# Optimization experiments

Measured on AMD Instinct MI355X. Metric: run time of the kernel, lower is better.

The kernel has to match this reference:

```python
import jax, jax.numpy as jnp
import numpy as np

N_NODES = 65536
IN_CH = 512
HIDDEN = 256          # hidden_channels[0] == encoder_hidden
OUT_CH = 8
NUM_GRAPHS = 32
MAX_LEN = 4096        # static pad bound (>= max per-graph length)
BN_EPS = 1e-5


def _make_batch_ids():
    # deterministic ragged per-graph lengths summing exactly to N_NODES
    rng = np.random.RandomState(0)
    d = rng.randint(-512, 512, size=NUM_GRAPHS)
    d[-1] -= d.sum()
    lengths = N_NODES // NUM_GRAPHS + d          # each in ~[1536, 2560] <= MAX_LEN
    return jnp.asarray(np.repeat(np.arange(NUM_GRAPHS), lengths), dtype=jnp.int32)


def setup_inputs() -> dict:
    key = jax.random.key(0)
    ks = jax.random.split(key, 12)
    f32 = jnp.float32
    inp = {
        'x_res': jax.random.normal(ks[0], (N_NODES, IN_CH), dtype=f32),
        'batch': _make_batch_ids(),
        # BatchNorm1d affine params
        'bn_gamma': jnp.ones((IN_CH,), f32),
        'bn_beta': jnp.zeros((IN_CH,), f32),
        # input2transformer: Linear(C,2H) GELU Linear(2H,H) GELU Linear(H,H)
        'W1': jax.random.normal(ks[1], (IN_CH, 2 * HIDDEN), f32) * (1.0 / np.sqrt(IN_CH)),
        'b1': jnp.zeros((2 * HIDDEN,), f32),
        'W2': jax.random.normal(ks[2], (2 * HIDDEN, HIDDEN), f32) * (1.0 / np.sqrt(2 * HIDDEN)),
        'b2': jnp.zeros((HIDDEN,), f32),
        'W3': jax.random.normal(ks[3], (HIDDEN, HIDDEN), f32) * (1.0 / np.sqrt(HIDDEN)),
        'b3': jnp.zeros((HIDDEN,), f32),
        # out_angles: Linear(encoder_hidden, out_ch) GELU DynamicTanh Tanh
        'Wo': jax.random.normal(ks[4], (HIDDEN, OUT_CH), f32) * (1.0 / np.sqrt(HIDDEN)),
        'bo': jnp.zeros((OUT_CH,), f32),
        'dyt_alpha': jnp.asarray(0.5, f32),
        'dyt_w': jnp.ones((OUT_CH,), f32),
        'dyt_b': jnp.zeros((OUT_CH,), f32),
    }
    return inp


def _forward(x_res, batch, bn_gamma, bn_beta, W1, b1, W2, b2, W3, b3,
             Wo, bo, dyt_alpha, dyt_w, dyt_b):
    # BatchNorm1d (training-mode batch stats, biased var), dropout is identity (eval)
    mu = jnp.mean(x_res, axis=0)
    var = jnp.mean((x_res - mu) ** 2, axis=0)
    x = (x_res - mu) * jax.lax.rsqrt(var + BN_EPS) * bn_gamma + bn_beta
    # input2transformer MLP (torch GELU default = exact erf)
    gelu = lambda t: jax.nn.gelu(t, approximate=False)
    x = gelu(x @ W1 + b1)
    x = gelu(x @ W2 + b2)
    x = x @ W3 + b3                                   # [N, HIDDEN]
    # ragged -> padded: scatter each node into (graph, position-in-graph)
    counts = jax.ops.segment_sum(jnp.ones_like(batch, dtype=jnp.int32), batch,
                                 num_segments=NUM_GRAPHS)
    offsets = jnp.concatenate([jnp.zeros((1,), jnp.int32),
                               jnp.cumsum(counts)[:-1].astype(jnp.int32)])
    pos = jnp.arange(N_NODES, dtype=jnp.int32) - offsets[batch]
    x_pad = jnp.zeros((NUM_GRAPHS, MAX_LEN, HIDDEN), x.dtype).at[batch, pos].set(x)
    z = jnp.transpose(x_pad, (1, 0, 2))               # [MAX_LEN, NUM_GRAPHS, HIDDEN] (stack dim=1)
    # out_angles head: Linear -> GELU -> DynamicTanh -> Tanh
    a = gelu(z @ Wo + bo)
    a = dyt_w * jnp.tanh(dyt_alpha * a) + dyt_b       # DynamicTanh (channels_last)
    return jnp.tanh(a)                                # [MAX_LEN, NUM_GRAPHS, OUT_CH]


def reference(x_res, batch, bn_gamma, bn_beta, W1, b1, W2, b2, W3, b3,
              Wo, bo, dyt_alpha, dyt_w, dyt_b):
    return _forward(x_res, batch, bn_gamma, bn_beta, W1, b1, W2, b2, W3, b3,
                    Wo, bo, dyt_alpha, dyt_w, dyt_b)
```

## Files before the change

kernel.cpp:

```cpp
#include <hip/hip_runtime.h>
#include <hip/hip_bf16.h>

#define N_NODES 65536
#define IN_CH 512
#define HIDDEN 256
#define OUT_CH 8
#define NUM_GRAPHS 32
#define MAX_LEN 4096
#define BN_EPS 1e-5f
#define BN_BLOCKS 2048

using short8  = __attribute__((ext_vector_type(8))) short;
using floatx4 = __attribute__((ext_vector_type(4))) float;
typedef unsigned int u32;
typedef unsigned short u16;

__device__ inline u16 f2b(float f) {
    u32 u = __float_as_uint(f);
    u += 0x7FFFu + ((u >> 16) & 1u);
    return (u16)(u >> 16);
}
__device__ inline float gelu_f(float x) {
    float z = x + 0.044715f * x * x * x;
    float e = __builtin_exp2f(-2.3022078f * z);
    return x * __builtin_amdgcn_rcpf(1.0f + e);
}
__device__ inline float tanh_f(float y) {
    y = fminf(fmaxf(y, -20.0f), 20.0f);
    float t = __builtin_exp2f(2.885390082f * y);
    return (t - 1.0f) * __builtin_amdgcn_rcpf(t + 1.0f);
}
__device__ inline void load_lds16(const void* g, void* l) {
    __builtin_amdgcn_global_load_lds(
        (const __attribute__((address_space(1))) u32*)g,
        (__attribute__((address_space(3))) u32*)l, 16, 0, 0);
}

__global__ __launch_bounds__(256) void statscast_k(const float* __restrict__ x,
                                                   u16* __restrict__ xb,
                                                   float4* __restrict__ partials) {
    __shared__ float4 sS[128];
    __shared__ float4 sQ[128];
    int tid = threadIdx.x;
    int half = tid >> 7;
    int c = tid & 127;
    const float4* x4 = (const float4*)x;
    uint2* xb2 = (uint2*)xb;
    float4 s = make_float4(0.f, 0.f, 0.f, 0.f);
    float4 q = make_float4(0.f, 0.f, 0.f, 0.f);
    int row0 = blockIdx.x * 32;
#pragma unroll
    for (int r = half; r < 32; r += 2) {
        size_t off = (size_t)(row0 + r) * 128 + c;
        float4 v = x4[off];
        s.x += v.x; s.y += v.y; s.z += v.z; s.w += v.w;
        q.x += v.x * v.x; q.y += v.y * v.y; q.z += v.z * v.z; q.w += v.w * v.w;
        uint2 o;
        o.x = (u32)f2b(v.x) | ((u32)f2b(v.y) << 16);
        o.y = (u32)f2b(v.z) | ((u32)f2b(v.w) << 16);
        xb2[off] = o;
    }
    if (half == 1) { sS[c] = s; sQ[c] = q; }
    __syncthreads();
    if (half == 0) {
        float4 s2 = sS[c], q2 = sQ[c];
        s.x += s2.x; s.y += s2.y; s.z += s2.z; s.w += s2.w;
        q.x += q2.x; q.y += q2.y; q.z += q2.z; q.w += q2.w;
        partials[(size_t)blockIdx.x * 256 + c * 2]     = make_float4(s.x, q.x, s.y, q.y);
        partials[(size_t)blockIdx.x * 256 + c * 2 + 1] = make_float4(s.z, q.z, s.w, q.w);
    }
}

__global__ __launch_bounds__(256) void bn_reduce_k(const float4* __restrict__ partials,
                                                   const float* __restrict__ gamma,
                                                   const float* __restrict__ beta,
                                                   float* __restrict__ scale,
                                                   float* __restrict__ shift) {
    __shared__ float4 sd[256];
    int tid = threadIdx.x;
    int g = blockIdx.x;
    float4 a = make_float4(0.f, 0.f, 0.f, 0.f);
    for (int r = tid; r < BN_BLOCKS; r += 256) {
        float4 v = partials[(size_t)r * 256 + g];
        a.x += v.x; a.y += v.y; a.z += v.z; a.w += v.w;
    }
    sd[tid] = a;
    __syncthreads();
    for (int st = 128; st > 0; st >>= 1) {
        if (tid < st) {
            float4 b = sd[tid + st];
            float4 m = sd[tid];
            m.x += b.x; m.y += b.y; m.z += b.z; m.w += b.w;
            sd[tid] = m;
        }
        __syncthreads();
    }
    if (tid == 0) {
        float4 t = sd[0];
        int c0 = g * 2, c1 = g * 2 + 1;
        const float inv = 1.0f / N_NODES;
        float mu0 = t.x * inv, var0 = t.y * inv - mu0 * mu0;
        float mu1 = t.z * inv, var1 = t.w * inv - mu1 * mu1;
        float sc0 = gamma[c0] * rsqrtf(var0 + BN_EPS);
        float sc1 = gamma[c1] * rsqrtf(var1 + BN_EPS);
        scale[c0] = sc0; shift[c0] = beta[c0] - mu0 * sc0;
        scale[c1] = sc1; shift[c1] = beta[c1] - mu1 * sc1;
    }
}

__global__ __launch_bounds__(256) void prep_k(const float* __restrict__ W1,
                                              const float* __restrict__ W2,
                                              const float* __restrict__ W3,
                                              const float* __restrict__ b1,
                                              const float* __restrict__ scale,
                                              const float* __restrict__ shift,
                                              u16* __restrict__ W1T,
                                              u16* __restrict__ W2T,
                                              u16* __restrict__ W3T,
                                              float* __restrict__ b1f,
                                              const int* __restrict__ batch,
                                              int* __restrict__ offsets,
                                              const float* __restrict__ bo,
                                              const float* __restrict__ alpha_p,
                                              const float* __restrict__ dyt_w,
                                              const float* __restrict__ dyt_b,
                                              float* __restrict__ out) {
    __shared__ int sof2[NUM_GRAPHS + 1];
    int bid = blockIdx.x;
    int tid = threadIdx.x;
    if (bid < 1792) {
        int idx = bid * 256 + tid;
        if (idx < 262144) {
            int k = idx >> 9, m = idx & 511;
            W1T[(size_t)m * 512 + k] = f2b(scale[k] * W1[idx]);
        } else if (idx < 262144 + 131072) {
            int i = idx - 262144;
            int k = i >> 8, m = i & 255;
            W2T[(size_t)m * 512 + k] = f2b(W2[i]);
        } else {
            int i = idx - 393216;
            int k = i >> 8, m = i & 255;
            W3T[(size_t)m * 256 + k] = f2b(W3[i]);
        }
        if (bid == 0 && tid < NUM_GRAPHS + 1) {
            int gph = tid;
            int lo = 0, hi = N_NODES;
            while (lo < hi) {
                int mid = (lo + hi) >> 1;
                if (batch[mid] < gph) lo = mid + 1; else hi = mid;
            }
            offsets[gph] = lo;
        }
    } else if (bid < 1794) {
        int m = (bid - 1792) * 256 + tid;
        float acc = b1[m];
#pragma unroll 16
        for (int k = 0; k < 512; ++k) acc += shift[k] * W1[k * 512 + m];
        b1f[m] = acc;
    } else {
        if (tid < NUM_GRAPHS + 1) {
            int target = tid;
            int lo = 0, hi = N_NODES;
            while (lo < hi) {
                int mid = (lo + hi) >> 1;
                if (batch[mid] < target) lo = mid + 1; else hi = mid;
            }
            sof2[tid] = lo;
        }
        __syncthreads();
        int idx = (bid - 1794) * 256 + tid;
        int g = idx & 31;
        int p = idx >> 5;
        if (p >= sof2[g + 1] - sof2[g]) {
            float alpha = alpha_p[0];
            float rv[8];
#pragma unroll
            for (int c = 0; c < 8; ++c) {
                float a = gelu_f(bo[c]);
                a = dyt_w[c] * tanh_f(alpha * a) + dyt_b[c];
                rv[c] = tanh_f(a);
            }
            float4* o = (float4*)(out + (size_t)idx * OUT_CH);
            o[0] = make_float4(rv[0], rv[1], rv[2], rv[3]);
            o[1] = make_float4(rv[4], rv[5], rv[6], rv[7]);
        }
    }
}

template <int DO_GELU, int NXB>
__global__ __launch_bounds__(512) void gemm_bt_k(const u16* __restrict__ A,
                                                 const u16* __restrict__ BT,
                                                 const float* __restrict__ bias,
                                                 u16* __restrict__ C,
                                                 int K, int M) {
    __shared__ __align__(16) u16 As[256 * 64];
    __shared__ __align__(16) u16 Bs[128 * 64];
    int tid = threadIdx.x;
    int lane = tid & 63;
    int bid = blockIdx.x;
    int xcd = bid & 7;
    int slot = bid >> 3;
    int rloc = slot / NXB;
    int colb = slot - rloc * NXB;
    int row0 = (xcd * 32 + rloc) * 256;
    int col0 = colb * 128;
    int wave = tid >> 6;
    int wr = (wave >> 1) * 64;
    int wc = (wave & 1) * 64;
    int l15 = lane & 15;
    int q = lane >> 4;

    floatx4 acc[4][4] = {};

    const int nkt = K >> 6;
    for (int kt = 0; kt < nkt; ++kt) {
        int k0 = kt << 6;
#pragma unroll
        for (int s = 0; s < 4; ++s) {
            int li = s * 512 + tid;
            int r = li >> 3;
            int g = li & 7;
            int gs = g ^ (r & 7);
            load_lds16(&A[(size_t)(row0 + r) * K + k0 + gs * 8], &As[li * 8]);
        }
#pragma unroll
        for (int s = 0; s < 2; ++s) {
            int li = s * 512 + tid;
            int r = li >> 3;
            int g = li & 7;
            int gs = g ^ (r & 7);
            load_lds16(&BT[(size_t)(col0 + r) * K + k0 + gs * 8], &Bs[li * 8]);
        }
        __syncthreads();
#pragma unroll
        for (int ks = 0; ks < 2; ++ks) {
            int gidx = ks * 4 + q;
            short8 af[4], bg[4];
#pragma unroll
            for (int i = 0; i < 4; ++i) {
                int row = wr + i * 16 + l15;
                af[i] = *(const short8*)&As[row * 64 + (gidx ^ (row & 7)) * 8];
            }
#pragma unroll
            for (int j = 0; j < 4; ++j) {
                int row = wc + j * 16 + l15;
                bg[j] = *(const short8*)&Bs[row * 64 + (gidx ^ (row & 7)) * 8];
            }
#pragma unroll
            for (int i = 0; i < 4; ++i)
#pragma unroll
                for (int j = 0; j < 4; ++j)
                    acc[i][j] = __builtin_amdgcn_mfma_f32_16x16x32_bf16(bg[j], af[i], acc[i][j], 0, 0, 0);
        }
        __syncthreads();
    }
#pragma unroll
    for (int i = 0; i < 4; ++i) {
        size_t rbase = (size_t)(row0 + wr + i * 16 + l15) * M;
#pragma unroll
        for (int j = 0; j < 4; ++j) {
            int c = col0 + wc + j * 16 + q * 4;
            float4 b4 = *(const float4*)&bias[c];
            float v0 = acc[i][j][0] + b4.x;
            float v1 = acc[i][j][1] + b4.y;
            float v2 = acc[i][j][2] + b4.z;
            float v3 = acc[i][j][3] + b4.w;
            if (DO_GELU) { v0 = gelu_f(v0); v1 = gelu_f(v1); v2 = gelu_f(v2); v3 = gelu_f(v3); }
            uint2 pk;
            pk.x = (u32)f2b(v0) | ((u32)f2b(v1) << 16);
            pk.y = (u32)f2b(v2) | ((u32)f2b(v3) << 16);
            *(uint2*)&C[rbase + c] = pk;
        }
    }
}

__global__ __launch_bounds__(512, 4) void gemm23h_k(const u16* __restrict__ A,
                                                    const u16* __restrict__ B2T,
                                                    const float* __restrict__ b2v,
                                                    const u16* __restrict__ W3T,
                                                    const float* __restrict__ b3v,
                                                    const float* __restrict__ Wo,
                                                    const float* __restrict__ bo,
                                                    const int* __restrict__ offsets,
                                                    const float* __restrict__ alpha_p,
                                                    const float* __restrict__ dyt_w,
                                                    const float* __restrict__ dyt_b,
                                                    float* __restrict__ out) {
    __shared__ __align__(16) u16 lds[32768];
    __shared__ float sWo[HIDDEN * OUT_CH];
    __shared__ int soff[NUM_GRAPHS + 1];
    int tid = threadIdx.x;
    int lane = tid & 63;
    int bid = blockIdx.x;
    int xcd = bid & 7;
    int slot = bid >> 3;
    int row0 = (xcd * 64 + slot) * 128;
    int wave = tid >> 6;
    int wr = (wave >> 2) * 64;
    int wc = (wave & 3) * 64;
    int l15 = lane & 15;
    int q = lane >> 4;

    ((float4*)sWo)[tid] = ((const float4*)Wo)[tid];
    if (tid < NUM_GRAPHS + 1) soff[tid] = offsets[tid];

    floatx4 acc[4][4] = {};

    const u16* pA[2];
    const u16* pB[4];
    int ldstA[2], ldstB[4];
#pragma unroll
    for (int s = 0; s < 2; ++s) {
        int li = s * 512 + tid;
        int r = li >> 3;
        int g = li & 7;
        int gs = g ^ (r & 7);
        pA[s] = A + (size_t)(row0 + r) * 512 + gs * 8;
        ldstA[s] = li * 8;
    }
#pragma unroll
    for (int s = 0; s < 4; ++s) {
        int li = s * 512 + tid;
        int r = li >> 3;
        int g = li & 7;
        int gs = g ^ (r & 7);
        pB[s] = B2T + (size_t)r * 512 + gs * 8;
        ldstB[s] = 8192 + li * 8;
    }

    for (int kt = 0; kt < 8; ++kt) {
        int k0 = kt << 6;
#pragma unroll
        for (int s = 0; s < 2; ++s) load_lds16(pA[s] + k0, &lds[ldstA[s]]);
#pragma unroll
        for (int s = 0; s < 4; ++s) load_lds16(pB[s] + k0, &lds[ldstB[s]]);
        __syncthreads();
#pragma unroll
        for (int ks = 0; ks < 2; ++ks) {
            int gidx = ks * 4 + q;
            short8 af[4], bg[4];
#pragma unroll
            for (int i = 0; i < 4; ++i) {
                int row = wr + i * 16 + l15;
                af[i] = *(const short8*)&lds[row * 64 + ((gidx ^ (row & 7)) << 3)];
            }
#pragma unroll
            for (int j = 0; j < 4; ++j) {
                int brow = wc + j * 16 + l15;
                bg[j] = *(const short8*)&lds[8192 + brow * 64 + ((gidx ^ (brow & 7)) << 3)];
            }
#pragma unroll
            for (int i = 0; i < 4; ++i)
#pragma unroll
                for (int j = 0; j < 4; ++j)
                    acc[i][j] = __builtin_amdgcn_mfma_f32_16x16x32_bf16(bg[j], af[i], acc[i][j], 0, 0, 0);
        }
        __syncthreads();
    }

#pragma unroll
    for (int i = 0; i < 4; ++i) {
        int row = wr + i * 16 + l15;
#pragma unroll
        for (int j = 0; j < 4; ++j) {
            int c = wc + j * 16 + q * 4;
            float4 b4 = *(const float4*)&b2v[c];
            float v0 = gelu_f(acc[i][j][0] + b4.x);
            float v1 = gelu_f(acc[i][j][1] + b4.y);
            float v2 = gelu_f(acc[i][j][2] + b4.z);
            float v3 = gelu_f(acc[i][j][3] + b4.w);
            uint2 pk;
            pk.x = (u32)f2b(v0) | ((u32)f2b(v1) << 16);
            pk.y = (u32)f2b(v2) | ((u32)f2b(v3) << 16);
            int gr = c >> 3;
            int addr = row * 256 + ((gr ^ (row & 7)) << 3) + (q & 1) * 4;
            *(uint2*)&lds[addr] = pk;
        }
    }
    __syncthreads();

#pragma unroll
    for (int i = 0; i < 4; ++i)
#pragma unroll
        for (int j = 0; j < 4; ++j)
            acc[i][j] = (floatx4){0.f, 0.f, 0.f, 0.f};

    for (int ks = 0; ks < 8; ++ks) {
        int gidx = ks * 4 + q;
        short8 af[4], bg[4];
#pragma unroll
        for (int j = 0; j < 4; ++j) {
            int colr = wc + j * 16 + l15;
            bg[j] = *(const short8*)&W3T[(size_t)colr * 256 + gidx * 8];
        }
#pragma unroll
        for (int i = 0; i < 4; ++i) {
            int row = wr + i * 16 + l15;
            af[i] = *(const short8*)&lds[row * 256 + ((gidx ^ (row & 7)) << 3)];
        }
        __builtin_amdgcn_s_setprio(1);
#pragma unroll
        for (int i = 0; i < 4; ++i)
#pragma unroll
            for (int j = 0; j < 4; ++j)
                acc[i][j] = __builtin_amdgcn_mfma_f32_16x16x32_bf16(bg[j], af[i], acc[i][j], 0, 0, 0);
        __builtin_amdgcn_s_setprio(0);
    }
    __syncthreads();

#pragma unroll
    for (int i = 0; i < 4; ++i) {
        int row = wr + i * 16 + l15;
#pragma unroll
        for (int j = 0; j < 4; ++j) {
            int c = wc + j * 16 + q * 4;
            float4 b4 = *(const float4*)&b3v[c];
            float v0 = acc[i][j][0] + b4.x;
            float v1 = acc[i][j][1] + b4.y;
            float v2 = acc[i][j][2] + b4.z;
            float v3 = acc[i][j][3] + b4.w;
            uint2 pk;
            pk.x = (u32)f2b(v0) | ((u32)f2b(v1) << 16);
            pk.y = (u32)f2b(v2) | ((u32)f2b(v3) << 16);
            int gr = c >> 3;
            int addr = row * 256 + ((gr ^ (row & 31)) << 3) + (q & 1) * 4;
            *(uint2*)&lds[addr] = pk;
        }
    }
    __syncthreads();

    {
        int r = tid >> 2;
        int cq = (tid & 3) * 2;
        int n = row0 + r;
        int lo = 0, hi = NUM_GRAPHS;
        while (hi - lo > 1) {
            int mid = (lo + hi) >> 1;
            if (soff[mid] <= n) lo = mid; else hi = mid;
        }
        int g = lo;
        int p = n - soff[g];
        float a0 = bo[cq], a1 = bo[cq + 1];
#pragma unroll 4
        for (int kk = 0; kk < 32; ++kk) {
            short8 h = *(const short8*)&lds[r * 256 + ((kk ^ (r & 31)) << 3)];
#pragma unroll
            for (int e = 0; e < 8; ++e) {
                float hv = __uint_as_float((u32)(u16)h[e] << 16);
                const float* w = &sWo[(kk * 8 + e) * 8 + cq];
                a0 += hv * w[0];
                a1 += hv * w[1];
            }
        }
        float alpha = alpha_p[0];
        float av[2] = {a0, a1};
        float rv[2];
#pragma unroll
        for (int c = 0; c < 2; ++c) {
            float a = gelu_f(av[c]);
            a = dyt_w[cq + c] * tanh_f(alpha * a) + dyt_b[cq + c];
            rv[c] = tanh_f(a);
        }
        *(float2*)&out[((size_t)(p * NUM_GRAPHS + g)) * 8 + cq] = make_float2(rv[0], rv[1]);
    }
}

extern "C" void kernel_launch(void* const* d_in, const int* in_sizes, int n_in,
                              void* d_out, int out_size, void* d_ws, size_t ws_size,
                              hipStream_t stream) {
    (void)in_sizes; (void)n_in; (void)out_size; (void)ws_size;
    const float* x_res = (const float*)d_in[0];
    const int*   batch = (const int*)d_in[1];
    const float* gamma = (const float*)d_in[2];
    const float* beta  = (const float*)d_in[3];
    const float* W1    = (const float*)d_in[4];
    const float* b1    = (const float*)d_in[5];
    const float* W2    = (const float*)d_in[6];
    const float* b2    = (const float*)d_in[7];
    const float* W3    = (const float*)d_in[8];
    const float* b3    = (const float*)d_in[9];
    const float* Wo    = (const float*)d_in[10];
    const float* bo    = (const float*)d_in[11];
    const float* alpha = (const float*)d_in[12];
    const float* dyt_w = (const float*)d_in[13];
    const float* dyt_b = (const float*)d_in[14];
    float* out = (float*)d_out;

    char* ws = (char*)d_ws;
    float* scale = (float*)(ws + 0);
    float* shift = (float*)(ws + 2048);
    float* b1f   = (float*)(ws + 4096);
    int*   offs  = (int*)(ws + 8192);
    u16* W1T = (u16*)(ws + 16384);
    u16* W2T = (u16*)(ws + 16384 + 524288);
    u16* W3T = (u16*)(ws + 16384 + 524288 + 262144);
    const size_t MB = 1024 * 1024;
    u16* xb = (u16*)(ws + 2 * MB);
    u16* h1 = (u16*)(ws + 66 * MB);
    float4* partials = (float4*)(ws + 66 * MB);

    statscast_k<<<BN_BLOCKS, 256, 0, stream>>>(x_res, xb, partials);
    bn_reduce_k<<<256, 256, 0, stream>>>(partials, gamma, beta, scale, shift);
    prep_k<<<2306, 256, 0, stream>>>(W1, W2, W3, b1, scale, shift,
                                     W1T, W2T, W3T, b1f, batch, offs,
                                     bo, alpha, dyt_w, dyt_b, out);
    gemm_bt_k<1, 4><<<1024, 512, 0, stream>>>(xb, W1T, b1f, h1, 512, 512);
    gemm23h_k<<<512, 512, 0, stream>>>(h1, W2T, b2, W3T, b3, Wo, bo, offs,
                                       alpha, dyt_w, dyt_b, out);
}
```

Measured before the change: 348.6 us.

## Move weight prep into stats kernel and shrink GEMM1 tile to 128x128

Work that does not depend on the BN statistics (W2/W3 transpose-cast, graph offsets and the padding-fill output) now runs as extra blocks inside the stats/cast kernel, so the prep kernel after the BN reduction only handles W1 and the folded bias. The first GEMM changes from 256x128 tiles with 512 threads to 128x128 tiles with 256 threads and twice as many blocks, for better occupancy and load balance. The goal is a shorter serial chain after the BN reduction and fuller GPU use in GEMM1. The cost is lower reuse of each B tile per block, since B is now loaded once per 128 rows instead of per 256.

Result: slower. 374.9 us (+7.6%).

```diff
diff --git a/kernel.cpp b/kernel.cpp
--- a/kernel.cpp
+++ b/kernel.cpp
@@ -38,36 +38,96 @@
 
 __global__ __launch_bounds__(256) void statscast_k(const float* __restrict__ x,
                                                    u16* __restrict__ xb,
-                                                   float4* __restrict__ partials) {
+                                                   float4* __restrict__ partials,
+                                                   const float* __restrict__ W2,
+                                                   const float* __restrict__ W3,
+                                                   u16* __restrict__ W2T,
+                                                   u16* __restrict__ W3T,
+                                                   const int* __restrict__ batch,
+                                                   int* __restrict__ offsets,
+                                                   const float* __restrict__ bo,
+                                                   const float* __restrict__ alpha_p,
+                                                   const float* __restrict__ dyt_w,
+                                                   const float* __restrict__ dyt_b,
+                                                   float* __restrict__ out) {
     __shared__ float4 sS[128];
     __shared__ float4 sQ[128];
+    __shared__ int sof2[NUM_GRAPHS + 1];
     int tid = threadIdx.x;
-    int half = tid >> 7;
-    int c = tid & 127;
-    const float4* x4 = (const float4*)x;
-    uint2* xb2 = (uint2*)xb;
-    float4 s = make_float4(0.f, 0.f, 0.f, 0.f);
-    float4 q = make_float4(0.f, 0.f, 0.f, 0.f);
-    int row0 = blockIdx.x * 32;
-#pragma unroll
-    for (int r = half; r < 32; r += 2) {
-        size_t off = (size_t)(row0 + r) * 128 + c;
-        float4 v = x4[off];
-        s.x += v.x; s.y += v.y; s.z += v.z; s.w += v.w;
-        q.x += v.x * v.x; q.y += v.y * v.y; q.z += v.z * v.z; q.w += v.w * v.w;
-        uint2 o;
-        o.x = (u32)f2b(v.x) | ((u32)f2b(v.y) << 16);
-        o.y = (u32)f2b(v.z) | ((u32)f2b(v.w) << 16);
-        xb2[off] = o;
-    }
-    if (half == 1) { sS[c] = s; sQ[c] = q; }
-    __syncthreads();
-    if (half == 0) {
-        float4 s2 = sS[c], q2 = sQ[c];
-        s.x += s2.x; s.y += s2.y; s.z += s2.z; s.w += s2.w;
-        q.x += q2.x; q.y += q2.y; q.z += q2.z; q.w += q2.w;
-        partials[(size_t)blockIdx.x * 256 + c * 2]     = make_float4(s.x, q.x, s.y, q.y);
-        partials[(size_t)blockIdx.x * 256 + c * 2 + 1] = make_float4(s.z, q.z, s.w, q.w);
+    int bid = blockIdx.x;
+    if (bid < 2048) {
+        int half = tid >> 7;
+        int c = tid & 127;
+        const float4* x4 = (const float4*)x;
+        uint2* xb2 = (uint2*)xb;
+        float4 s = make_float4(0.f, 0.f, 0.f, 0.f);
+        float4 q = make_float4(0.f, 0.f, 0.f, 0.f);
+        int row0 = bid * 32;
+#pragma unroll
+        for (int r = half; r < 32; r += 2) {
+            size_t off = (size_t)(row0 + r) * 128 + c;
+            float4 v = x4[off];
+            s.x += v.x; s.y += v.y; s.z += v.z; s.w += v.w;
+            q.x += v.x * v.x; q.y += v.y * v.y; q.z += v.z * v.z; q.w += v.w * v.w;
+            uint2 o;
+            o.x = (u32)f2b(v.x) | ((u32)f2b(v.y) << 16);
+            o.y = (u32)f2b(v.z) | ((u32)f2b(v.w) << 16);
+            xb2[off] = o;
+        }
+        if (half == 1) { sS[c] = s; sQ[c] = q; }
+        __syncthreads();
+        if (half == 0) {
+            float4 s2 = sS[c], q2 = sQ[c];
+            s.x += s2.x; s.y += s2.y; s.z += s2.z; s.w += s2.w;
+            q.x += q2.x; q.y += q2.y; q.z += q2.z; q.w += q2.w;
+            partials[(size_t)bid * 256 + c * 2]     = make_float4(s.x, q.x, s.y, q.y);
+            partials[(size_t)bid * 256 + c * 2 + 1] = make_float4(s.z, q.z, s.w, q.w);
+        }
+    } else if (bid < 2560) {
+        int i = (bid - 2048) * 256 + tid;
+        int k = i >> 8, m = i & 255;
+        W2T[(size_t)m * 512 + k] = f2b(W2[i]);
+    } else if (bid < 2816) {
+        int i = (bid - 2560) * 256 + tid;
+        int k = i >> 8, m = i & 255;
+        W3T[(size_t)m * 256 + k] = f2b(W3[i]);
+    } else if (bid < 3328) {
+        if (tid < NUM_GRAPHS + 1) {
+            int target = tid;
+            int lo = 0, hi = N_NODES;
+            while (lo < hi) {
+                int mid = (lo + hi) >> 1;
+                if (batch[mid] < target) lo = mid + 1; else hi = mid;
+            }
+            sof2[tid] = lo;
+        }
+        __syncthreads();
+        int idx = (bid - 2816) * 256 + tid;
+        int g = idx & 31;
+        int p = idx >> 5;
+        if (p >= sof2[g + 1] - sof2[g]) {
+            float alpha = alpha_p[0];
+            float rv[8];
+#pragma unroll
+            for (int c = 0; c < 8; ++c) {
+                float a = gelu_f(bo[c]);
+                a = dyt_w[c] * tanh_f(alpha * a) + dyt_b[c];
+                rv[c] = tanh_f(a);
+            }
+            float4* o = (float4*)(out + (size_t)idx * OUT_CH);
+            o[0] = make_float4(rv[0], rv[1], rv[2], rv[3]);
+            o[1] = make_float4(rv[4], rv[5], rv[6], rv[7]);
+        }
+    } else {
+        if (tid < NUM_GRAPHS + 1) {
+            int gph = tid;
+            int lo = 0, hi = N_NODES;
+            while (lo < hi) {
+                int mid = (lo + hi) >> 1;
+                if (batch[mid] < gph) lo = mid + 1; else hi = mid;
+            }
+            offsets[gph] = lo;
+        }
     }
 }
 
@@ -108,92 +168,34 @@
     }
 }
 
-__global__ __launch_bounds__(256) void prep_k(const float* __restrict__ W1,
-                                              const float* __restrict__ W2,
-                                              const float* __restrict__ W3,
-                                              const float* __restrict__ b1,
-                                              const float* __restrict__ scale,
-                                              const float* __restrict__ shift,
-                                              u16* __restrict__ W1T,
-                                              u16* __restrict__ W2T,
-                                              u16* __restrict__ W3T,
-                                              float* __restrict__ b1f,
-                                              const int* __restrict__ batch,
-                                              int* __restrict__ offsets,
-                                              const float* __restrict__ bo,
-                                              const float* __restrict__ alpha_p,
-                                              const float* __restrict__ dyt_w,
-                                              const float* __restrict__ dyt_b,
-                                              float* __restrict__ out) {
-    __shared__ int sof2[NUM_GRAPHS + 1];
+__global__ __launch_bounds__(256) void prep1_k(const float* __restrict__ W1,
+                                               const float* __restrict__ b1,
+                                               const float* __restrict__ scale,
+                                               const float* __restrict__ shift,
+                                               u16* __restrict__ W1T,
+                                               float* __restrict__ b1f) {
     int bid = blockIdx.x;
     int tid = threadIdx.x;
-    if (bid < 1792) {
+    if (bid < 1024) {
         int idx = bid * 256 + tid;
-        if (idx < 262144) {
-            int k = idx >> 9, m = idx & 511;
-            W1T[(size_t)m * 512 + k] = f2b(scale[k] * W1[idx]);
-        } else if (idx < 262144 + 131072) {
-            int i = idx - 262144;
-            int k = i >> 8, m = i & 255;
-            W2T[(size_t)m * 512 + k] = f2b(W2[i]);
-        } else {
-            int i = idx - 393216;
-            int k = i >> 8, m = i & 255;
-            W3T[(size_t)m * 256 + k] = f2b(W3[i]);
-        }
-        if (bid == 0 && tid < NUM_GRAPHS + 1) {
-            int gph = tid;
-            int lo = 0, hi = N_NODES;
-            while (lo < hi) {
-                int mid = (lo + hi) >> 1;
-                if (batch[mid] < gph) lo = mid + 1; else hi = mid;
-            }
-            offsets[gph] = lo;
-        }
-    } else if (bid < 1794) {
-        int m = (bid - 1792) * 256 + tid;
+        int k = idx >> 9, m = idx & 511;
+        W1T[(size_t)m * 512 + k] = f2b(scale[k] * W1[idx]);
+    } else {
+        int m = (bid - 1024) * 256 + tid;
         float acc = b1[m];
 #pragma unroll 16
         for (int k = 0; k < 512; ++k) acc += shift[k] * W1[k * 512 + m];
         b1f[m] = acc;
-    } else {
-        if (tid < NUM_GRAPHS + 1) {
-            int target = tid;
-            int lo = 0, hi = N_NODES;
-            while (lo < hi) {
-                int mid = (lo + hi) >> 1;
-                if (batch[mid] < target) lo = mid + 1; else hi = mid;
-            }
-            sof2[tid] = lo;
-        }
-        __syncthreads();
-        int idx = (bid - 1794) * 256 + tid;
-        int g = idx & 31;
-        int p = idx >> 5;
-        if (p >= sof2[g + 1] - sof2[g]) {
-            float alpha = alpha_p[0];
-            float rv[8];
-#pragma unroll
-            for (int c = 0; c < 8; ++c) {
-                float a = gelu_f(bo[c]);
-                a = dyt_w[c] * tanh_f(alpha * a) + dyt_b[c];
-                rv[c] = tanh_f(a);
-            }
-            float4* o = (float4*)(out + (size_t)idx * OUT_CH);
-            o[0] = make_float4(rv[0], rv[1], rv[2], rv[3]);
-            o[1] = make_float4(rv[4], rv[5], rv[6], rv[7]);
-        }
     }
 }
 
 template <int DO_GELU, int NXB>
-__global__ __launch_bounds__(512) void gemm_bt_k(const u16* __restrict__ A,
+__global__ __launch_bounds__(256) void gemm_bt_k(const u16* __restrict__ A,
                                                  const u16* __restrict__ BT,
                                                  const float* __restrict__ bias,
                                                  u16* __restrict__ C,
                                                  int K, int M) {
-    __shared__ __align__(16) u16 As[256 * 64];
+    __shared__ __align__(16) u16 As[128 * 64];
     __shared__ __align__(16) u16 Bs[128 * 64];
     int tid = threadIdx.x;
     int lane = tid & 63;
@@ -202,7 +204,7 @@
     int slot = bid >> 3;
     int rloc = slot / NXB;
     int colb = slot - rloc * NXB;
-    int row0 = (xcd * 32 + rloc) * 256;
+    int row0 = (xcd * 64 + rloc) * 128;
     int col0 = colb * 128;
     int wave = tid >> 6;
     int wr = (wave >> 1) * 64;
@@ -217,15 +219,15 @@
         int k0 = kt << 6;
 #pragma unroll
         for (int s = 0; s < 4; ++s) {
-            int li = s * 512 + tid;
+            int li = s * 256 + tid;
             int r = li >> 3;
             int g = li & 7;
             int gs = g ^ (r & 7);
             load_lds16(&A[(size_t)(row0 + r) * K + k0 + gs * 8], &As[li * 8]);
         }
 #pragma unroll
-        for (int s = 0; s < 2; ++s) {
-            int li = s * 512 + tid;
+        for (int s = 0; s < 4; ++s) {
+            int li = s * 256 + tid;
             int r = li >> 3;
             int g = li & 7;
             int gs = g ^ (r & 7);
@@ -499,12 +501,11 @@
     u16* h1 = (u16*)(ws + 66 * MB);
     float4* partials = (float4*)(ws + 66 * MB);
 
-    statscast_k<<<BN_BLOCKS, 256, 0, stream>>>(x_res, xb, partials);
+    statscast_k<<<3329, 256, 0, stream>>>(x_res, xb, partials, W2, W3, W2T, W3T,
+                                          batch, offs, bo, alpha, dyt_w, dyt_b, out);
     bn_reduce_k<<<256, 256, 0, stream>>>(partials, gamma, beta, scale, shift);
-    prep_k<<<2306, 256, 0, stream>>>(W1, W2, W3, b1, scale, shift,
-                                     W1T, W2T, W3T, b1f, batch, offs,
-                                     bo, alpha, dyt_w, dyt_b, out);
-    gemm_bt_k<1, 4><<<1024, 512, 0, stream>>>(xb, W1T, b1f, h1, 512, 512);
+    prep1_k<<<1026, 256, 0, stream>>>(W1, b1, scale, shift, W1T, b1f);
+    gemm_bt_k<1, 4><<<2048, 256, 0, stream>>>(xb, W1T, b1f, h1, 512, 512);
     gemm23h_k<<<512, 512, 0, stream>>>(h1, W2T, b2, W3T, b3, Wo, bo, offs,
                                        alpha, dyt_w, dyt_b, out);
 }
```
